# Kernel tuning notes

Hardware: AMD Instinct MI355X
Metric: run time of the kernel (lower is better)

## Reference

```python
import jax, jax.numpy as jnp
import numpy as np


def setup_inputs() -> dict:
    key = jax.random.key(0)
    k1, k2, k3 = jax.random.split(key, 3)
    num, c_in, c_out, din, dout = 64, 4, 4, 2, 2
    sx = sy = 256
    nx, ny = sx // 2 + sx % 2, sy // 2 + sy % 2
    x = jax.random.normal(k1, (num, c_in, din, sx, sy), dtype=jnp.float32)
    # weight tensor: (c_in, c_out, nx, ny, din, din, din, din, dout)
    tensors = jax.random.normal(k2, (c_in, c_out, nx, ny, din, din, din, din, dout), dtype=jnp.float32)
    bias = jax.random.normal(k3, (c_out, nx, ny, dout), dtype=jnp.float32) * 1e-8
    return {"x": x, "tensors": tensors, "bias": bias}


def reference(x, tensors, bias):
    # x: (n, c, d, sx, sy); tensors: (c, p, nx, ny, d, d, d, d, o); bias: (p, nx, ny, o)
    n, c, d, sx, sy = x.shape
    nx = sx // 2 + sx % 2
    ny = sy // 2 + sy % 2
    # boundary-clamped 2x2 patch indices (matches min(2*i+1, s-1) in the source)
    ix0 = jnp.arange(nx) * 2
    ix1 = jnp.minimum(ix0 + 1, sx - 1)
    iy0 = jnp.arange(ny) * 2
    iy1 = jnp.minimum(iy0 + 1, sy - 1)
    # four corner pixels of every 2x2 patch, each (n, c, d, nx, ny)
    a = x[:, :, :, ix0][:, :, :, :, iy0]  # (2i,   2j)
    b = x[:, :, :, ix1][:, :, :, :, iy0]  # (2i+1, 2j)
    e = x[:, :, :, ix0][:, :, :, :, iy1]  # (2i,   2j+1)
    f = x[:, :, :, ix1][:, :, :, :, iy1]  # (2i+1, 2j+1)
    # outer product of the four local features -> (n, c, nx, ny, d^4)
    patch = jnp.einsum('ncixy,ncjxy,nckxy,nclxy->ncxyijkl', a, b, e, f)
    patch = patch.reshape(n, c, nx, ny, d ** 4)
    c_out, dout = tensors.shape[1], tensors.shape[-1]
    w = tensors.reshape(c, c_out, nx, ny, d ** 4, dout)
    # per-position contraction over c_in and the d^4 patch index
    out = jnp.einsum('ncxyq,cpxyqo->npoxy', patch, w)
    out = out + bias.transpose(0, 3, 1, 2)[None]  # (1, p, o, nx, ny)
    return out
```

## Files before the change

kernel.cpp:

```cpp
#include <hip/hip_runtime.h>

#define NUMN 64
#define CIN 4
#define COUT 4
#define SX 256
#define SY 256
#define NXX 128
#define NYY 128
#define YTILE 8
#define NSPLIT 2
#define NPER (NUMN / NSPLIT)
#define PLANE (SX * SY)

__global__ __launch_bounds__(64, 4)
void ttn_kernel(const float* __restrict__ x, const float* __restrict__ w,
                const float* __restrict__ bias, float* __restrict__ out)
{
    __shared__ float lds[4 * 256];

    const int bid = blockIdx.x;
    const int xi = bid % NXX;
    const int yt = (bid / NXX) % (NYY / YTILE);
    const int ns = bid / (NXX * (NYY / YTILE));

    const int tid = threadIdx.x;
    const int yl  = tid & (YTILE - 1);
    const int po  = tid >> 3;
    const int p   = po >> 1;
    const int o   = po & 1;
    const int y   = yt * YTILE + yl;

    float wr[CIN][16];
#pragma unroll
    for (int c = 0; c < CIN; ++c) {
        const float4* wp4 = (const float4*)(w +
            ((size_t)(((c * COUT + p) * NXX + xi) * NYY + y)) * 32);
#pragma unroll
        for (int j = 0; j < 8; ++j) {
            const float4 v = wp4[j];
            wr[c][2 * j]     = o ? v.y : v.x;
            wr[c][2 * j + 1] = o ? v.w : v.z;
        }
    }
    const float bv = bias[(((p * NXX + xi) * NYY + y) * 2) + o];

    const size_t nstr = (size_t)CIN * 2 * PLANE;
    const size_t ostr = (size_t)COUT * 2 * NXX * NYY;

    const int mc = tid >> 2;
    const int cd = mc >> 1;
    const int rr = mc & 1;
    const int j0 = (tid & 3) * 4;

    const float* xs = x + (size_t)(ns * NPER) * nstr
                        + (size_t)cd * PLANE
                        + (size_t)(2 * xi + rr) * SY + yt * 16 + j0;
    float* ob = out + (size_t)(ns * NPER) * ostr
                    + (size_t)po * (NXX * NYY) + xi * NYY + y;
    float* lb = &lds[0];

    asm volatile("s_waitcnt vmcnt(0)" ::: "memory");

#define STAGE(nn, slot)                                                        \
    __builtin_amdgcn_global_load_lds(                                          \
        (const __attribute__((address_space(1))) void*)(xs + (size_t)(nn) * nstr), \
        (__attribute__((address_space(3))) void*)(lb + ((slot) << 8)), 16, 0, 0)

    STAGE(0, 0);
    STAGE(1, 1);
    STAGE(2, 2);

    for (int n = 0; n < NPER; ++n) {
        const int ns3 = (n + 3 < NPER) ? (n + 3) : (NPER - 1);
        STAGE(ns3, ns3 & 3);

        if      (n >= 3) asm volatile("s_waitcnt vmcnt(6)" ::: "memory");
        else if (n == 2) asm volatile("s_waitcnt vmcnt(5)" ::: "memory");
        else if (n == 1) asm volatile("s_waitcnt vmcnt(4)" ::: "memory");
        else             asm volatile("s_waitcnt vmcnt(3)" ::: "memory");

        const float2* b2 = (const float2*)(lb + ((n & 3) << 8));
        float acc = bv;
#pragma unroll
        for (int c = 0; c < CIN; ++c) {
            const float2 ae0 = b2[c * 32 +      yl];
            const float2 bf0 = b2[c * 32 +  8 + yl];
            const float2 ae1 = b2[c * 32 + 16 + yl];
            const float2 bf1 = b2[c * 32 + 24 + yl];
            const float a0 = ae0.x, e0 = ae0.y, b0 = bf0.x, f0 = bf0.y;
            const float a1 = ae1.x, e1 = ae1.y, b1 = bf1.x, f1 = bf1.y;
            const float ef00 = e0*f0, ef01 = e0*f1, ef10 = e1*f0, ef11 = e1*f1;
            const float ab00 = a0*b0, ab01 = a0*b1, ab10 = a1*b0, ab11 = a1*b1;
            const float* wq = wr[c];
            float t;
            t = ef00*wq[ 0] + ef01*wq[ 1] + ef10*wq[ 2] + ef11*wq[ 3];  acc += ab00 * t;
            t = ef00*wq[ 4] + ef01*wq[ 5] + ef10*wq[ 6] + ef11*wq[ 7];  acc += ab01 * t;
            t = ef00*wq[ 8] + ef01*wq[ 9] + ef10*wq[10] + ef11*wq[11];  acc += ab10 * t;
            t = ef00*wq[12] + ef01*wq[13] + ef10*wq[14] + ef11*wq[15];  acc += ab11 * t;
        }
        ob[(size_t)n * ostr] = acc;
    }
#undef STAGE
}

extern "C" void kernel_launch(void* const* d_in, const int* in_sizes, int n_in,
                              void* d_out, int out_size, void* d_ws, size_t ws_size,
                              hipStream_t stream) {
    const float* x    = (const float*)d_in[0];
    const float* w    = (const float*)d_in[1];
    const float* bias = (const float*)d_in[2];
    float* out = (float*)d_out;

    const int grid = NXX * (NYY / YTILE) * NSPLIT;
    ttn_kernel<<<grid, 64, 0, stream>>>(x, w, bias, out);
}
```

Baseline: 236.8 us.

## Expand blocks to full y-row with 1024 threads and barrier-synced shared LDS staging

Each block now covers a whole row of 128 y positions for all output channels, using 1024 threads (16 waves) instead of 64. Each wave stages one 256-float segment of the input row into a 4-slot LDS ring, and a block barrier is placed before each step so every wave sees data loaded by the others. This makes the global loads for a full image row fully contiguous and cuts the grid to 256 blocks. In exchange it adds per-iteration barriers, uses much more LDS, and leaves fewer blocks to spread across the CUs.

```diff
diff --git a/kernel.cpp b/kernel.cpp
--- a/kernel.cpp
+++ b/kernel.cpp
@@ -7,28 +7,28 @@
 #define SY 256
 #define NXX 128
 #define NYY 128
-#define YTILE 8
 #define NSPLIT 2
 #define NPER (NUMN / NSPLIT)
 #define PLANE (SX * SY)
+#define SLOTF 4096
 
-__global__ __launch_bounds__(64, 4)
+__global__ __launch_bounds__(1024, 4)
 void ttn_kernel(const float* __restrict__ x, const float* __restrict__ w,
                 const float* __restrict__ bias, float* __restrict__ out)
 {
-    __shared__ float lds[4 * 256];
+    __shared__ float lds[4 * SLOTF];
 
     const int bid = blockIdx.x;
     const int xi = bid % NXX;
-    const int yt = (bid / NXX) % (NYY / YTILE);
-    const int ns = bid / (NXX * (NYY / YTILE));
+    const int ns = bid / NXX;
 
     const int tid = threadIdx.x;
-    const int yl  = tid & (YTILE - 1);
-    const int po  = tid >> 3;
+    const int wv  = tid >> 6;
+    const int l   = tid & 63;
+    const int po  = tid >> 7;
     const int p   = po >> 1;
     const int o   = po & 1;
-    const int y   = yt * YTILE + yl;
+    const int y   = tid & 127;
 
     float wr[CIN][16];
 #pragma unroll
@@ -47,14 +47,9 @@
     const size_t nstr = (size_t)CIN * 2 * PLANE;
     const size_t ostr = (size_t)COUT * 2 * NXX * NYY;
 
-    const int mc = tid >> 2;
-    const int cd = mc >> 1;
-    const int rr = mc & 1;
-    const int j0 = (tid & 3) * 4;
-
     const float* xs = x + (size_t)(ns * NPER) * nstr
-                        + (size_t)cd * PLANE
-                        + (size_t)(2 * xi + rr) * SY + yt * 16 + j0;
+                        + (size_t)(wv >> 1) * PLANE
+                        + (size_t)(2 * xi + (wv & 1)) * SY + 4 * l;
     float* ob = out + (size_t)(ns * NPER) * ostr
                     + (size_t)po * (NXX * NYY) + xi * NYY + y;
     float* lb = &lds[0];
@@ -64,29 +59,32 @@
 #define STAGE(nn, slot)                                                        \
     __builtin_amdgcn_global_load_lds(                                          \
         (const __attribute__((address_space(1))) void*)(xs + (size_t)(nn) * nstr), \
-        (__attribute__((address_space(3))) void*)(lb + ((slot) << 8)), 16, 0, 0)
+        (__attribute__((address_space(3))) void*)(lb + ((slot) << 12) + (wv << 8)), \
+        16, 0, 0)
 
     STAGE(0, 0);
     STAGE(1, 1);
     STAGE(2, 2);
 
     for (int n = 0; n < NPER; ++n) {
+        if      (n >= 3) asm volatile("s_waitcnt vmcnt(5)" ::: "memory");
+        else if (n == 2) asm volatile("s_waitcnt vmcnt(4)" ::: "memory");
+        else if (n == 1) asm volatile("s_waitcnt vmcnt(3)" ::: "memory");
+        else             asm volatile("s_waitcnt vmcnt(2)" ::: "memory");
+        __builtin_amdgcn_s_barrier();
+        asm volatile("" ::: "memory");
+
         const int ns3 = (n + 3 < NPER) ? (n + 3) : (NPER - 1);
         STAGE(ns3, ns3 & 3);
 
-        if      (n >= 3) asm volatile("s_waitcnt vmcnt(6)" ::: "memory");
-        else if (n == 2) asm volatile("s_waitcnt vmcnt(5)" ::: "memory");
-        else if (n == 1) asm volatile("s_waitcnt vmcnt(4)" ::: "memory");
-        else             asm volatile("s_waitcnt vmcnt(3)" ::: "memory");
-
-        const float2* b2 = (const float2*)(lb + ((n & 3) << 8));
+        const float2* b2 = (const float2*)(lb + ((n & 3) << 12));
         float acc = bv;
 #pragma unroll
         for (int c = 0; c < CIN; ++c) {
-            const float2 ae0 = b2[c * 32 +      yl];
-            const float2 bf0 = b2[c * 32 +  8 + yl];
-            const float2 ae1 = b2[c * 32 + 16 + yl];
-            const float2 bf1 = b2[c * 32 + 24 + yl];
+            const float2 ae0 = b2[c * 512 +       y];
+            const float2 bf0 = b2[c * 512 + 128 + y];
+            const float2 ae1 = b2[c * 512 + 256 + y];
+            const float2 bf1 = b2[c * 512 + 384 + y];
             const float a0 = ae0.x, e0 = ae0.y, b0 = bf0.x, f0 = bf0.y;
             const float a1 = ae1.x, e1 = ae1.y, b1 = bf1.x, f1 = bf1.y;
             const float ef00 = e0*f0, ef01 = e0*f1, ef10 = e1*f0, ef11 = e1*f1;
@@ -111,6 +109,6 @@
     const float* bias = (const float*)d_in[2];
     float* out = (float*)d_out;
 
-    const int grid = NXX * (NYY / YTILE) * NSPLIT;
-    ttn_kernel<<<grid, 64, 0, stream>>>(x, w, bias, out);
+    const int grid = NXX * NSPLIT;
+    ttn_kernel<<<grid, 1024, 0, stream>>>(x, w, bias, out);
 }
```

Measured after the change: 244.3 us. +3.2%, slower.
